# Kernel tuning notes

Measured on AMD Instinct MI355X. Metric: run time of the kernel, lower is better.

Reference implementation:

```python
import jax, jax.numpy as jnp
import numpy as np

COS_EPS = 1e-8  # torch F.cosine_similarity eps


def setup_inputs() -> dict:
    key = jax.random.key(0)
    k1, k2 = jax.random.split(key)
    N, D = 4096, 1024
    features = jax.random.normal(k1, (N, D), dtype=jnp.float32)
    y = jax.random.randint(k2, (N,), 0, 100, dtype=jnp.int64)
    return {"features": features, "y": y}


def reference(features, y):
    y = y.reshape(-1)
    # shared building blocks: row norms and Gram matrix (one GEMM)
    sq = jnp.sum(features * features, axis=-1)            # [N]
    gram = features @ features.T                           # [N, N]
    # Euclidean cdist via ||a||^2 + ||b||^2 - 2 a.b, safe sqrt (grad 0 at 0)
    d2 = sq[:, None] + sq[None, :] - 2.0 * gram
    pos = d2 > 0
    dist = jnp.where(pos, jnp.sqrt(jnp.where(pos, d2, 1.0)), 0.0)
    # cosine similarity with torch-style eps clamp on norms
    norm = jnp.maximum(jnp.sqrt(sq), COS_EPS)              # [N]
    sim = gram / (norm[:, None] * norm[None, :])
    # (eq - ~eq) = 2*eq - 1 signed mask
    eq = (y[:, None] == y[None, :])
    sgn = jnp.where(eq, 1.0, -1.0).astype(features.dtype)
    # loss = sum(sgn * dist) + sum(-sgn * sim)
    return jnp.sum(sgn * dist) - jnp.sum(sgn * sim)
```

## Files before the change

kernel.cpp:

```cpp
#include <hip/hip_runtime.h>
#include <stdint.h>

typedef __attribute__((ext_vector_type(4)))  int   i32x4;
typedef __attribute__((ext_vector_type(8)))  int   i32x8;
typedef __attribute__((ext_vector_type(16))) float f32x16;

#define NROWS 4096
#define DDIM  1024
#define NKT   16
#define NB    32
#define NBLK  528
#define COS_EPS 1e-8f
#define SCL   0x7F7F7F7F

__device__ __forceinline__ void gload16(const uint8_t* g, uint8_t* l) {
  __builtin_amdgcn_global_load_lds(
      (const __attribute__((address_space(1))) uint32_t*)g,
      (__attribute__((address_space(3))) uint32_t*)l, 16, 0, 0);
}

__device__ __forceinline__ i32x8 cat8(i32x4 lo, i32x4 hi) {
  i32x8 r;
  r[0] = lo[0]; r[1] = lo[1]; r[2] = lo[2]; r[3] = lo[3];
  r[4] = hi[0]; r[5] = hi[1]; r[6] = hi[2]; r[7] = hi[3];
  return r;
}

extern "C" __global__ void __launch_bounds__(256) prep_kernel(
    const float* __restrict__ F, uint8_t* __restrict__ Fb,
    float* __restrict__ sq, float* __restrict__ rn, float* __restrict__ out) {
  if (blockIdx.x == 0 && threadIdx.x == 0) out[0] = 0.f;
  const int row  = blockIdx.x * 4 + (threadIdx.x >> 6);
  const int lane = threadIdx.x & 63;
  const float4* src = (const float4*)(F + (size_t)row * DDIM + lane * 16);
  float4 v[4];
#pragma unroll
  for (int i = 0; i < 4; ++i) v[i] = src[i];
  float s = 0.f;
#pragma unroll
  for (int i = 0; i < 4; ++i)
    s += v[i].x * v[i].x + v[i].y * v[i].y + v[i].z * v[i].z + v[i].w * v[i].w;
  uint32_t d[4];
#pragma unroll
  for (int i = 0; i < 4; ++i) {
    int w = __builtin_amdgcn_cvt_pk_fp8_f32(v[i].x, v[i].y, 0, false);
    w = __builtin_amdgcn_cvt_pk_fp8_f32(v[i].z, v[i].w, w, true);
    d[i] = (uint32_t)w;
  }
  *(uint4*)(Fb + (size_t)row * DDIM + lane * 16) = make_uint4(d[0], d[1], d[2], d[3]);
#pragma unroll
  for (int off = 32; off; off >>= 1) s += __shfl_down(s, off);
  if (lane == 0) {
    sq[row] = s;
    rn[row] = 1.0f / fmaxf(sqrtf(s), COS_EPS);
  }
}

extern "C" __global__ void __launch_bounds__(512, 4) gram_kernel(
    const uint8_t* __restrict__ Fb, const float* __restrict__ sq,
    const float* __restrict__ rn, const int* __restrict__ y,
    float* __restrict__ out) {
  __shared__ __align__(16) uint8_t As[3][8192];
  __shared__ __align__(16) uint8_t Bs[3][8192];
  __shared__ float wsum[8];

  int s = (int)(blockIdx.x & 7) * 66 + (int)(blockIdx.x >> 3);
  int bi = 0, rem0 = s;
  while (rem0 >= NB - bi) { rem0 -= NB - bi; ++bi; }
  const int bj = bi + rem0;
  const bool diag = (bi == bj);

  const int tid  = threadIdx.x;
  const int lane = tid & 63;
  const int wid  = tid >> 6;
  const int wr   = wid >> 2;
  const int wc   = wid & 3;
  const int kg   = lane >> 5;
  const int r32  = lane & 31;

  const int hc   = (tid & 7) ^ ((tid >> 3) & 7);
  const int srow = 2 * (tid >> 3) + ((hc >> 2) & 1);
  const int scol = (hc & 3) * 16;
  const uint8_t* gA = Fb + (size_t)(bi * 128 + srow) * DDIM + scol;
  const uint8_t* gB = Fb + (size_t)(bj * 128 + srow) * DDIM + scol;
  uint8_t* ldsA = &As[0][0] + tid * 16;
  uint8_t* ldsB = &Bs[0][0] + tid * 16;

  int offA[2], offB1;
#pragma unroll
  for (int mt = 0; mt < 2; ++mt) {
    const int R = wr * 64 + mt * 32 + r32;
    const int u = R >> 1, h = R & 1;
    offA[mt] = u * 128 + (((h << 2) + 2 * kg) ^ (u & 7)) * 16;
  }
  {
    const int R = wc * 32 + r32;
    const int u = R >> 1, h = R & 1;
    offB1 = u * 128 + (((h << 2) + 2 * kg) ^ (u & 7)) * 16;
  }

  f32x16 acc[2] = {};

#define STAGE(kt2) do {                                                     \
    const int _sl = (kt2) % 3;                                              \
    gload16(gA + (kt2) * 64, ldsA + _sl * 8192);                            \
    gload16(gB + (kt2) * 64, ldsB + _sl * 8192);                            \
  } while (0)

  STAGE(0); STAGE(1);
  asm volatile("s_waitcnt vmcnt(2)");
  __builtin_amdgcn_s_barrier();
  __builtin_amdgcn_sched_barrier(0);

#pragma unroll 1
  for (int kt = 0; kt < NKT; ++kt) {
    const uint8_t* sa = &As[0][0] + (kt % 3) * 8192;
    const uint8_t* sb = &Bs[0][0] + (kt % 3) * 8192;

    const i32x8 A0 = cat8(*(const i32x4*)(sa + offA[0]),
                          *(const i32x4*)(sa + (offA[0] ^ 16)));
    const i32x8 A1 = cat8(*(const i32x4*)(sa + offA[1]),
                          *(const i32x4*)(sa + (offA[1] ^ 16)));
    const i32x8 B0 = cat8(*(const i32x4*)(sb + offB1),
                          *(const i32x4*)(sb + (offB1 ^ 16)));

    if (kt + 2 < NKT) STAGE(kt + 2);

    acc[0] = __builtin_amdgcn_mfma_scale_f32_32x32x64_f8f6f4(
        A0, B0, acc[0], 0, 0, 0, SCL, 0, SCL);
    acc[1] = __builtin_amdgcn_mfma_scale_f32_32x32x64_f8f6f4(
        A1, B0, acc[1], 0, 0, 0, SCL, 0, SCL);

    if (kt + 2 < NKT)       asm volatile("s_waitcnt vmcnt(2)");
    else if (kt == NKT - 2) asm volatile("s_waitcnt vmcnt(0)");
    if (kt < NKT - 1) {
      __builtin_amdgcn_s_barrier();
      __builtin_amdgcn_sched_barrier(0);
    }
  }

#undef STAGE

  const int gj = bj * 128 + wc * 32 + r32;
  const float sqj = sq[gj], rnj = rn[gj];
  const int yj = y[gj];
  float lsum = 0.f;
#pragma unroll
  for (int mt = 0; mt < 2; ++mt) {
#pragma unroll
    for (int e = 0; e < 16; ++e) {
      const int gi = bi * 128 + wr * 64 + mt * 32 + (e & 3) + 8 * (e >> 2) + 4 * kg;
      const float g  = acc[mt][e];
      const float d2 = sq[gi] + sqj - 2.0f * g;
      const float dist = d2 > 0.f ? sqrtf(d2) : 0.f;
      const float sim  = g * rn[gi] * rnj;
      const float sgn  = (y[gi] == yj) ? 1.0f : -1.0f;
      float wgt;
      if (diag) wgt = (gj > gi) ? 2.0f : ((gj == gi) ? 1.0f : 0.0f);
      else      wgt = 2.0f;
      lsum += wgt * sgn * (dist - sim);
    }
  }
#pragma unroll
  for (int off = 32; off; off >>= 1) lsum += __shfl_down(lsum, off);
  if (lane == 0) wsum[wid] = lsum;
  __syncthreads();
  if (tid == 0) {
    float t = 0.f;
#pragma unroll
    for (int i = 0; i < 8; ++i) t += wsum[i];
    atomicAdd(out, t);
  }
}

extern "C" void kernel_launch(void* const* d_in, const int* in_sizes, int n_in,
                              void* d_out, int out_size, void* d_ws, size_t ws_size,
                              hipStream_t stream) {
  const float* F = (const float*)d_in[0];
  const int*   y = (const int*)d_in[1];
  float* out = (float*)d_out;

  uint8_t* Fb = (uint8_t*)d_ws;
  float*  sq = (float*)((char*)d_ws + (size_t)NROWS * DDIM);
  float*  rn = sq + NROWS;

  prep_kernel<<<NROWS / 4, 256, 0, stream>>>(F, Fb, sq, rn, out);
  gram_kernel<<<NBLK, 512, 0, stream>>>(Fb, sq, rn, y, out);
}
```

Measured before the change: 34.16 us.

## Deepen LDS ring to four stages and prefetch fragments into registers

The LDS ring buffer grows from three to four stages, so global loads are issued three tiles ahead. The loop is unrolled by two with ping-pong register sets, so LDS fragment reads for the next k-tile are issued before the MFMAs of the current tile. This is meant to hide LDS read latency and global load latency behind matrix-core work. In exchange, LDS use rises to 64KB per block and register pressure goes up, which may reduce occupancy under the 512x4 launch bound.

Measured after the change: 39.83 us. +16.6%, slower.

```diff
diff --git a/kernel.cpp b/kernel.cpp
--- a/kernel.cpp
+++ b/kernel.cpp
@@ -60,8 +60,8 @@
     const uint8_t* __restrict__ Fb, const float* __restrict__ sq,
     const float* __restrict__ rn, const int* __restrict__ y,
     float* __restrict__ out) {
-  __shared__ __align__(16) uint8_t As[3][8192];
-  __shared__ __align__(16) uint8_t Bs[3][8192];
+  __shared__ __align__(16) uint8_t As[4][8192];
+  __shared__ __align__(16) uint8_t Bs[4][8192];
   __shared__ float wsum[8];
 
   int s = (int)(blockIdx.x & 7) * 66 + (int)(blockIdx.x >> 3);
@@ -86,60 +86,81 @@
   uint8_t* ldsA = &As[0][0] + tid * 16;
   uint8_t* ldsB = &Bs[0][0] + tid * 16;
 
-  int offA[2], offB1;
-#pragma unroll
-  for (int mt = 0; mt < 2; ++mt) {
-    const int R = wr * 64 + mt * 32 + r32;
-    const int u = R >> 1, h = R & 1;
-    offA[mt] = u * 128 + (((h << 2) + 2 * kg) ^ (u & 7)) * 16;
-  }
+  int offA0, offA1, offB1;
   {
-    const int R = wc * 32 + r32;
-    const int u = R >> 1, h = R & 1;
+    int R = wr * 64 + 0 * 32 + r32, u = R >> 1, h = R & 1;
+    offA0 = u * 128 + (((h << 2) + 2 * kg) ^ (u & 7)) * 16;
+    R = wr * 64 + 1 * 32 + r32; u = R >> 1; h = R & 1;
+    offA1 = u * 128 + (((h << 2) + 2 * kg) ^ (u & 7)) * 16;
+    R = wc * 32 + r32; u = R >> 1; h = R & 1;
     offB1 = u * 128 + (((h << 2) + 2 * kg) ^ (u & 7)) * 16;
   }
 
   f32x16 acc[2] = {};
+  i32x4 p0_0, p0_1, p0_2, p0_3, p0_4, p0_5;
+  i32x4 p1_0, p1_1, p1_2, p1_3, p1_4, p1_5;
 
 #define STAGE(kt2) do {                                                     \
-    const int _sl = (kt2) % 3;                                              \
+    const int _sl = (kt2) & 3;                                              \
     gload16(gA + (kt2) * 64, ldsA + _sl * 8192);                            \
     gload16(gB + (kt2) * 64, ldsB + _sl * 8192);                            \
   } while (0)
 
-  STAGE(0); STAGE(1);
+#define RD(set, kt1) do {                                                   \
+    const uint8_t* _sa = &As[(kt1) & 3][0];                                 \
+    const uint8_t* _sb = &Bs[(kt1) & 3][0];                                 \
+    p##set##_0 = *(const i32x4*)(_sa + offA0);                              \
+    p##set##_1 = *(const i32x4*)(_sa + (offA0 ^ 16));                       \
+    p##set##_2 = *(const i32x4*)(_sa + offA1);                              \
+    p##set##_3 = *(const i32x4*)(_sa + (offA1 ^ 16));                       \
+    p##set##_4 = *(const i32x4*)(_sb + offB1);                              \
+    p##set##_5 = *(const i32x4*)(_sb + (offB1 ^ 16));                       \
+  } while (0)
+
+#define MFMA2(set) do {                                                     \
+    const i32x8 _A0 = cat8(p##set##_0, p##set##_1);                         \
+    const i32x8 _A1 = cat8(p##set##_2, p##set##_3);                         \
+    const i32x8 _B0 = cat8(p##set##_4, p##set##_5);                         \
+    acc[0] = __builtin_amdgcn_mfma_scale_f32_32x32x64_f8f6f4(               \
+        _A0, _B0, acc[0], 0, 0, 0, SCL, 0, SCL);                            \
+    acc[1] = __builtin_amdgcn_mfma_scale_f32_32x32x64_f8f6f4(               \
+        _A1, _B0, acc[1], 0, 0, 0, SCL, 0, SCL);                            \
+  } while (0)
+
+#define ITER(S, N, k) do {                                                  \
+    if ((k) + 3 < NKT) STAGE((k) + 3);                                      \
+    if ((k) + 1 < NKT) {                                                    \
+      RD(N, (k) + 1);                                                       \
+      asm volatile("s_waitcnt lgkmcnt(6)");                                 \
+    } else {                                                                \
+      asm volatile("s_waitcnt lgkmcnt(0)");                                 \
+    }                                                                       \
+    __builtin_amdgcn_sched_barrier(0);                                      \
+    MFMA2(S);                                                               \
+    if ((k) + 3 < NKT)        asm volatile("s_waitcnt vmcnt(2)");           \
+    else if ((k) == NKT - 3)  asm volatile("s_waitcnt vmcnt(0)");           \
+    if ((k) < NKT - 1) {                                                    \
+      __builtin_amdgcn_s_barrier();                                         \
+      __builtin_amdgcn_sched_barrier(0);                                    \
+    }                                                                       \
+  } while (0)
+
+  STAGE(0); STAGE(1); STAGE(2);
   asm volatile("s_waitcnt vmcnt(2)");
   __builtin_amdgcn_s_barrier();
   __builtin_amdgcn_sched_barrier(0);
+  RD(0, 0);
 
 #pragma unroll 1
-  for (int kt = 0; kt < NKT; ++kt) {
-    const uint8_t* sa = &As[0][0] + (kt % 3) * 8192;
-    const uint8_t* sb = &Bs[0][0] + (kt % 3) * 8192;
-
-    const i32x8 A0 = cat8(*(const i32x4*)(sa + offA[0]),
-                          *(const i32x4*)(sa + (offA[0] ^ 16)));
-    const i32x8 A1 = cat8(*(const i32x4*)(sa + offA[1]),
-                          *(const i32x4*)(sa + (offA[1] ^ 16)));
-    const i32x8 B0 = cat8(*(const i32x4*)(sb + offB1),
-                          *(const i32x4*)(sb + (offB1 ^ 16)));
-
-    if (kt + 2 < NKT) STAGE(kt + 2);
-
-    acc[0] = __builtin_amdgcn_mfma_scale_f32_32x32x64_f8f6f4(
-        A0, B0, acc[0], 0, 0, 0, SCL, 0, SCL);
-    acc[1] = __builtin_amdgcn_mfma_scale_f32_32x32x64_f8f6f4(
-        A1, B0, acc[1], 0, 0, 0, SCL, 0, SCL);
-
-    if (kt + 2 < NKT)       asm volatile("s_waitcnt vmcnt(2)");
-    else if (kt == NKT - 2) asm volatile("s_waitcnt vmcnt(0)");
-    if (kt < NKT - 1) {
-      __builtin_amdgcn_s_barrier();
-      __builtin_amdgcn_sched_barrier(0);
-    }
+  for (int kt = 0; kt < NKT; kt += 2) {
+    ITER(0, 1, kt);
+    ITER(1, 0, kt + 1);
   }
 
 #undef STAGE
+#undef RD
+#undef MFMA2
+#undef ITER
 
   const int gj = bj * 128 + wc * 32 + r32;
   const float sqj = sq[gj], rnj = rn[gj];
```
